# Optimization experiments

Measured on AMD Instinct MI355X. Metric: run time of the kernel, lower is better.

The kernel has to match this reference:

```python
import jax, jax.numpy as jnp
import numpy as np

D_MODEL = 1024
N_HEAD = 16
HEAD_SIZE = D_MODEL // N_HEAD
LAYER_ID = 12
N_LAYER = 24
HEAD_SIZE_DIVISOR = 8
TM_DIM = 32   # TIME_MIX_EXTRA_DIM
TD_DIM = 64   # TIME_DECAY_EXTRA_DIM
B, T = 4, 1024
EPS = 1e-5 * HEAD_SIZE_DIVISOR ** 2


def setup_inputs() -> dict:
    key = jax.random.key(0)
    ks = jax.random.split(key, 12)
    C = D_MODEL
    r0 = LAYER_ID / (N_LAYER - 1)
    r1 = 1.0 - LAYER_ID / N_LAYER
    ddd = np.arange(C, dtype=np.float64) / C
    time_maa_x = (1.0 - ddd ** r1).astype(np.float32)
    time_maa_w = (1.0 - ddd ** r1).astype(np.float32)
    time_maa_k = (1.0 - ddd ** r1).astype(np.float32)
    time_maa_v = (1.0 - (ddd ** r1 + 0.3 * r0)).astype(np.float32)
    time_maa_r = (1.0 - ddd ** (0.5 * r1)).astype(np.float32)
    time_maa_g = (1.0 - ddd ** (0.5 * r1)).astype(np.float32)
    n = np.arange(C, dtype=np.float64)
    time_decay = (-6.0 + 5.0 * (n / (C - 1)) ** (0.7 + 1.3 * r0)).astype(np.float32)
    zig = ((n + 1) % 3 - 1) * 0.1
    time_faaaa = (r0 * (1 - n / (C - 1)) + zig).astype(np.float32).reshape(N_HEAD, HEAD_SIZE)
    s = 1.0 / np.sqrt(C)
    inp = {
        "x": jax.random.normal(ks[0], (B, T, C), jnp.float32),
        "time_maa_x": jnp.asarray(time_maa_x),
        "time_maa_w": jnp.asarray(time_maa_w),
        "time_maa_k": jnp.asarray(time_maa_k),
        "time_maa_v": jnp.asarray(time_maa_v),
        "time_maa_r": jnp.asarray(time_maa_r),
        "time_maa_g": jnp.asarray(time_maa_g),
        "time_maa_w1": jax.random.uniform(ks[1], (C, TM_DIM * 5), jnp.float32, -0.01, 0.01),
        "time_maa_w2": jax.random.uniform(ks[2], (5, TM_DIM, C), jnp.float32, -0.01, 0.01),
        "time_decay": jnp.asarray(time_decay),
        "time_decay_w1": jax.random.uniform(ks[3], (C, TD_DIM), jnp.float32, -0.01, 0.01),
        "time_decay_w2": jax.random.uniform(ks[4], (TD_DIM, C), jnp.float32, -0.01, 0.01),
        "time_faaaa": jnp.asarray(time_faaaa),
        "W_r": jax.random.normal(ks[5], (C, C), jnp.float32) * s,
        "W_k": jax.random.normal(ks[6], (C, C), jnp.float32) * s,
        "W_v": jax.random.normal(ks[7], (C, C), jnp.float32) * s,
        "W_g": jax.random.normal(ks[8], (C, C), jnp.float32) * s,
        "W_o": jax.random.normal(ks[9], (C, C), jnp.float32) * s,
        "ln_gamma": jnp.ones((C,), jnp.float32),
        "ln_beta": jnp.zeros((C,), jnp.float32),
    }
    return inp


def _wkv6(r, k, v, w, u):
    # r,k,v,w: (B,T,H,K); u: (H,K). Sequential data-dependent linear attention.
    Bc, Tc, H, K = r.shape
    wdec = jnp.exp(-jnp.exp(w))  # decay in (0,1)

    def step(S, inp):
        r_t, k_t, v_t, wd_t = inp           # each (B,H,K)
        kv = k_t[:, :, :, None] * v_t[:, :, None, :]   # (B,H,K,K) key x value
        y = jnp.einsum('bhk,bhkj->bhj', r_t, S + u[None, :, :, None] * kv)
        S = S * wd_t[:, :, :, None] + kv    # decay along key dim, then accumulate
        return S, y

    S0 = jnp.zeros((Bc, H, K, K), r.dtype)
    xs = (jnp.swapaxes(r, 0, 1), jnp.swapaxes(k, 0, 1),
          jnp.swapaxes(v, 0, 1), jnp.swapaxes(wdec, 0, 1))
    _, ys = jax.lax.scan(step, S0, xs)      # ys: (T,B,H,K)
    return jnp.swapaxes(ys, 0, 1).reshape(Bc, Tc, H * K)


def reference(x, time_maa_x, time_maa_w, time_maa_k, time_maa_v, time_maa_r,
              time_maa_g, time_maa_w1, time_maa_w2, time_decay, time_decay_w1,
              time_decay_w2, time_faaaa, W_r, W_k, W_v, W_g, W_o, ln_gamma, ln_beta):
    Bc, Tc, C = x.shape
    H, K = N_HEAD, HEAD_SIZE
    # token shift: state[t] = x[t-1], zero at t=0
    xs = jnp.pad(x, ((0, 0), (1, 0), (0, 0)))[:, :-1]
    xx = xs - x
    # LoRA-style data-dependent mixing coefficients
    xxx = x + xx * time_maa_x
    m = jnp.tanh(xxx @ time_maa_w1).reshape(Bc, Tc, 5, TM_DIM)
    m = jnp.einsum('btfe,fec->fbtc', m, time_maa_w2)  # (5,B,T,C)
    mw, mk, mv, mr, mg = m[0], m[1], m[2], m[3], m[4]
    xw = x + xx * (time_maa_w + mw)
    xk = x + xx * (time_maa_k + mk)
    xv = x + xx * (time_maa_v + mv)
    xr = x + xx * (time_maa_r + mr)
    xg = x + xx * (time_maa_g + mg)
    r = xr @ W_r
    k = xk @ W_k
    v = xv @ W_v
    g = jax.nn.silu(xg @ W_g)
    w = time_decay + jnp.tanh(xw @ time_decay_w1) @ time_decay_w2
    y = _wkv6(r.reshape(Bc, Tc, H, K), k.reshape(Bc, Tc, H, K),
              v.reshape(Bc, Tc, H, K), w.reshape(Bc, Tc, H, K), time_faaaa)
    # GroupNorm with H groups over channel dim (per (b,t) position)
    yg = y.reshape(Bc, Tc, H, K)
    mu = jnp.mean(yg, axis=-1, keepdims=True)
    var = jnp.mean((yg - mu) ** 2, axis=-1, keepdims=True)
    yn = ((yg - mu) / jnp.sqrt(var + EPS)).reshape(Bc, Tc, C)
    yn = yn * ln_gamma + ln_beta
    return (yn * g) @ W_o
```

## Files before the change

### kernel.cpp

```cpp
#include <hip/hip_runtime.h>

#define Bb 4
#define Tt 1024
#define Cc 1024
#define Hh 16
#define BT (Bb*Tt)
#define CHUNK 32
#define NCH (Tt/CHUNK)

typedef unsigned int uint;
typedef unsigned short u16;
typedef __bf16 bf16x8 __attribute__((ext_vector_type(8)));
typedef float f32x4 __attribute__((ext_vector_type(4)));
typedef const __attribute__((address_space(1))) uint GU;
typedef __attribute__((address_space(3))) uint LU;

__device__ __forceinline__ float blo(uint u) { return __uint_as_float(u << 16); }
__device__ __forceinline__ float bhi(uint u) { return __uint_as_float(u & 0xffff0000u); }
__device__ __forceinline__ float b2f(u16 u) { return __uint_as_float(((uint)u) << 16); }
__device__ __forceinline__ u16 f2b(float f) {
  uint u = __float_as_uint(f);
  return (u16)((u + 0x7fffu + ((u >> 16) & 1u)) >> 16);
}

__global__ __launch_bounds__(256) void prep_xxx(const float* __restrict__ x,
    const float* __restrict__ maa_x, u16* __restrict__ xxx)
{
  int idx = blockIdx.x*256 + threadIdx.x;
  int c4 = idx & 255;
  int bt = idx >> 8;
  int t = bt & (Tt-1);
  float4 xc = ((const float4*)x)[idx];
  float4 xp = make_float4(0.f,0.f,0.f,0.f);
  if (t > 0) xp = ((const float4*)x)[idx - 256];
  float4 mx = ((const float4*)maa_x)[c4];
  ushort4 o;
  o.x = f2b(fmaf(xp.x - xc.x, mx.x, xc.x));
  o.y = f2b(fmaf(xp.y - xc.y, mx.y, xc.y));
  o.z = f2b(fmaf(xp.z - xc.z, mx.z, xc.z));
  o.w = f2b(fmaf(xp.w - xc.w, mx.w, xc.w));
  ((ushort4*)xxx)[idx] = o;
}

__global__ __launch_bounds__(256) void mix_mfma(
    const float* __restrict__ x, const u16* __restrict__ m1b,
    const u16* __restrict__ w2T,
    const float* __restrict__ maa_w, const float* __restrict__ maa_k,
    const float* __restrict__ maa_v, const float* __restrict__ maa_r,
    const float* __restrict__ maa_g,
    u16* __restrict__ xw, u16* __restrict__ xk, u16* __restrict__ xv,
    u16* __restrict__ xr, u16* __restrict__ xg)
{
  const int tid = threadIdx.x;
  const int lane = tid & 63;
  const int wv = tid >> 6;
  const int sid = blockIdx.x*4 + wv;
  const int rs = sid >> 4, cs = sid & 15;
  const int r0 = rs*16, c0 = cs*64;
  const int fr = lane & 15, kc = lane >> 4;

  float xc[4][4], xd[4][4];
  #pragma unroll
  for (int n = 0; n < 4; ++n) {
    int col = c0 + n*16 + fr;
    #pragma unroll
    for (int q = 0; q < 4; ++q) {
      int row = r0 + kc*4 + q;
      size_t o = (size_t)row*Cc + col;
      float v = x[o];
      float p = ((row & (Tt-1)) != 0) ? x[o - Cc] : 0.f;
      xc[n][q] = v;
      xd[n][q] = p - v;
    }
  }

  const u16* aB = m1b + (size_t)(r0 + fr)*160 + kc*8;
  u16* const outs[5] = {xw, xk, xv, xr, xg};
  const float* const maas[5] = {maa_w, maa_k, maa_v, maa_r, maa_g};

  #pragma unroll
  for (int f = 0; f < 5; ++f) {
    bf16x8 af = *(const bf16x8*)(aB + f*32);
    f32x4 acc[4];
    #pragma unroll
    for (int n = 0; n < 4; ++n) {
      bf16x8 bg = *(const bf16x8*)(w2T + (size_t)(c0 + n*16 + fr)*160 + f*32 + kc*8);
      acc[n] = __builtin_amdgcn_mfma_f32_16x16x32_bf16(af, bg, f32x4{0.f,0.f,0.f,0.f}, 0, 0, 0);
    }
    const float* __restrict__ ma = maas[f];
    u16* __restrict__ op = outs[f];
    #pragma unroll
    for (int n = 0; n < 4; ++n) {
      int col = c0 + n*16 + fr;
      float mv = ma[col];
      #pragma unroll
      for (int q = 0; q < 4; ++q) {
        int row = r0 + kc*4 + q;
        op[(size_t)row*Cc + col] = f2b(fmaf(xd[n][q], mv + acc[n][q], xc[n][q]));
      }
    }
  }
}

struct WPair { const float* s; u16* d; int K; int N; };
struct WPack { WPair p[9]; };

__global__ __launch_bounds__(256) void transW(WPack wp) {
  WPair pr = wp.p[blockIdx.z];
  int c0 = blockIdx.x*32, r0 = blockIdx.y*32;
  if (c0 >= pr.N || r0 >= pr.K) return;
  __shared__ float tile[32][33];
  int tc = threadIdx.x & 31, tr = threadIdx.x >> 5;
  #pragma unroll
  for (int p = 0; p < 4; ++p)
    tile[tr + p*8][tc] = pr.s[(size_t)(r0 + tr + p*8)*pr.N + c0 + tc];
  __syncthreads();
  #pragma unroll
  for (int p = 0; p < 4; ++p) {
    int n = tr + p*8;
    pr.d[(size_t)(c0 + n)*pr.K + r0 + tc] = f2b(tile[tc][n]);
  }
}

template<bool OUTF32>
__device__ __forceinline__ void mfma_core(
    const u16* __restrict__ A, const u16* __restrict__ Bt,
    void* __restrict__ Cout, const float* __restrict__ bias,
    int K, int N, int act)
{
  __shared__ __align__(16) u16 lds[2][2][128*32];
  const int tid = threadIdx.x;
  const int lane = tid & 63;
  const int wv = __builtin_amdgcn_readfirstlane(tid >> 6);

  const int nby8 = gridDim.y >> 3;
  const int i_lin = blockIdx.y * gridDim.x + blockIdx.x;
  const int cx = i_lin & 7, rest = i_lin >> 3;
  const int bm = (cx * nby8 + rest % nby8) * 128;
  const int bn = (rest / nby8) * 128;

  const int wm = (wv >> 1) * 64;
  const int wn = (wv & 1) * 64;
  const int kc = lane >> 4;
  const int fr = lane & 15;

  const int srow = wv*16 + (lane >> 2);
  const int ssw  = (srow >> 1) & 3;
  const int scol = ((lane & 3) ^ ssw) * 8;
  const size_t aoff = (size_t)(bm + srow) * K + scol;
  const size_t boff = (size_t)(bn + srow) * K + scol;

#define STAGE(bufi, kt) do { \
    size_t ko_ = (size_t)(kt) * 32; \
    __builtin_amdgcn_global_load_lds((GU*)(A + aoff + ko_), \
        (LU*)&lds[bufi][0][wv*512], 16, 0, 0); \
    __builtin_amdgcn_global_load_lds((GU*)(A + aoff + (size_t)64*K + ko_), \
        (LU*)&lds[bufi][0][wv*512 + 64*32], 16, 0, 0); \
    __builtin_amdgcn_global_load_lds((GU*)(Bt + boff + ko_), \
        (LU*)&lds[bufi][1][wv*512], 16, 0, 0); \
    __builtin_amdgcn_global_load_lds((GU*)(Bt + boff + (size_t)64*K + ko_), \
        (LU*)&lds[bufi][1][wv*512 + 64*32], 16, 0, 0); \
  } while(0)

  int ard[4], brd[4];
  #pragma unroll
  for (int m = 0; m < 4; ++m) {
    int ra = wm + m*16 + fr;
    int rb = wn + m*16 + fr;
    ard[m] = ra*32 + (kc ^ ((ra >> 1) & 3))*8;
    brd[m] = rb*32 + (kc ^ ((rb >> 1) & 3))*8;
  }

  f32x4 acc[4][4];
  #pragma unroll
  for (int m = 0; m < 4; ++m)
    #pragma unroll
    for (int n = 0; n < 4; ++n)
      acc[m][n] = f32x4{0.f, 0.f, 0.f, 0.f};

  const int NK = K >> 5;
  STAGE(0, 0);
  __syncthreads();
  int buf = 0;
  for (int kt = 0; kt < NK; ++kt) {
    if (kt + 1 < NK) STAGE(buf^1, kt+1);
    bf16x8 af[4], bg[4];
    #pragma unroll
    for (int m = 0; m < 4; ++m) af[m] = *(const bf16x8*)&lds[buf][0][ard[m]];
    #pragma unroll
    for (int n = 0; n < 4; ++n) bg[n] = *(const bf16x8*)&lds[buf][1][brd[n]];
    #pragma unroll
    for (int m = 0; m < 4; ++m)
      #pragma unroll
      for (int n = 0; n < 4; ++n)
        acc[m][n] = __builtin_amdgcn_mfma_f32_16x16x32_bf16(af[m], bg[n], acc[m][n], 0, 0, 0);
    __syncthreads();
    buf ^= 1;
  }
#undef STAGE

  const int orow = bm + wm + (lane >> 4) * 4;
  const int ocol = bn + wn + fr;
  #pragma unroll
  for (int m = 0; m < 4; ++m) {
    #pragma unroll
    for (int n = 0; n < 4; ++n) {
      int col = ocol + n*16;
      if (col < N) {
        float bs = bias ? bias[col] : 0.f;
        #pragma unroll
        for (int q = 0; q < 4; ++q) {
          float vv = acc[m][n][q] + bs;
          if (act == 1) vv = tanhf(vv);
          else if (act == 2) vv = vv / (1.f + __expf(-vv));
          else if (act == 3) vv = __expf(-__expf(vv));
          else if (act == 4) vv = __expf(vv);
          size_t off = (size_t)(orow + m*16 + q) * N + col;
          if (OUTF32) ((float*)Cout)[off] = vv;
          else ((u16*)Cout)[off] = f2b(vv);
        }
      }
    }
  }
}

template<int ACT, bool OUTF32>
__global__ __launch_bounds__(256) void gemm_mfma(
    const u16* __restrict__ A, const u16* __restrict__ Bt,
    void* __restrict__ Cout, const float* __restrict__ bias, int K, int N)
{
  mfma_core<OUTF32>(A, Bt, Cout, bias, K, N, ACT);
}

struct GPack { const u16* A[4]; const u16* B[4]; u16* C[4]; };

#define VMW(n) asm volatile("s_waitcnt vmcnt(" #n ")" ::: "memory")
#define LGKM0() asm volatile("s_waitcnt lgkmcnt(0)" ::: "memory")
#define SCHB() __builtin_amdgcn_sched_barrier(0)
#define HBAR() __builtin_amdgcn_s_barrier()

__global__ __launch_bounds__(512) void gemm_rkvg256(GPack gp) {
  __shared__ __align__(16) u16 lds[2][2][2][8192];
  const int z = blockIdx.z;
  const u16* __restrict__ Ap  = gp.A[z];
  const u16* __restrict__ Btp = gp.B[z];
  u16* __restrict__ Cp = gp.C[z];
  const int act = (z == 3) ? 2 : 0;

  const int tid = threadIdx.x;
  const int lane = tid & 63;
  const int wv = __builtin_amdgcn_readfirstlane(tid >> 6);

  const int i_lin = blockIdx.y * gridDim.x + blockIdx.x;
  const int tile = (i_lin & 7) * 8 + (i_lin >> 3);
  const int bm = (tile >> 2) * 256;
  const int bn = (tile & 3) * 256;

  const int wm = (wv >> 2) * 128;
  const int wn = (wv & 3) * 64;
  const int kc = lane >> 4;
  const int fr = lane & 15;

  const int srow0 = (wv*2 + 0)*16 + (lane >> 2);
  const int srow1 = (wv*2 + 1)*16 + (lane >> 2);
  const int sc0 = ((lane & 3) ^ ((srow0 >> 1) & 3)) * 8;
  const int sc1 = ((lane & 3) ^ ((srow1 >> 1) & 3)) * 8;
  const size_t aoff0 = (size_t)(bm + srow0)*Cc + sc0;
  const size_t aoff1 = (size_t)(bm + srow1)*Cc + sc1;
  const size_t boff0 = (size_t)(bn + srow0)*Cc + sc0;
  const size_t boff1 = (size_t)(bn + srow1)*Cc + sc1;

  int ard[8], brd[4];
  #pragma unroll
  for (int mh = 0; mh < 2; ++mh)
    #pragma unroll
    for (int mf = 0; mf < 4; ++mf) {
      int r = wm + mh*64 + mf*16 + fr;
      ard[mh*4+mf] = r*32 + (kc ^ ((r >> 1) & 3))*8;
    }
  #pragma unroll
  for (int nf = 0; nf < 4; ++nf) {
    int r = wn + nf*16 + fr;
    brd[nf] = r*32 + (kc ^ ((r >> 1) & 3))*8;
  }

  f32x4 acc[8][4];
  #pragma unroll
  for (int m = 0; m < 8; ++m)
    #pragma unroll
    for (int n = 0; n < 4; ++n)
      acc[m][n] = f32x4{0.f, 0.f, 0.f, 0.f};

#define STG256(DB, MAT, KH, kt, off0, off1, src) do { \
    u16* dst_ = &lds[(DB)][(MAT)][(KH)][wv*1024]; \
    __builtin_amdgcn_global_load_lds((GU*)((src) + (off0) + (size_t)(kt)*64 + (KH)*32), \
        (LU*)dst_, 16, 0, 0); \
    __builtin_amdgcn_global_load_lds((GU*)((src) + (off1) + (size_t)(kt)*64 + (KH)*32), \
        (LU*)(dst_ + 512), 16, 0, 0); \
  } while(0)

#define PH256(cur, KH, MH, LOADB, STMAT, STKH, DOSTAGE, VMTOK) do { \
    _Pragma("unroll") \
    for (int mf = 0; mf < 4; ++mf) \
      af[mf] = *(const bf16x8*)&lds[(cur)][0][KH][ard[(MH)*4+mf]]; \
    if (LOADB) { \
      _Pragma("unroll") \
      for (int nf = 0; nf < 4; ++nf) \
        bg[nf] = *(const bf16x8*)&lds[(cur)][1][KH][brd[nf]]; \
    } \
    if (DOSTAGE) { \
      if ((STMAT) == 0) STG256((cur)^1, 0, STKH, t+1, aoff0, aoff1, Ap); \
      else              STG256((cur)^1, 1, STKH, t+1, boff0, boff1, Btp); \
    } \
    VMTOK; \
    SCHB(); \
    HBAR(); \
    LGKM0(); \
    SCHB(); \
    __builtin_amdgcn_s_setprio(1); \
    _Pragma("unroll") \
    for (int mf = 0; mf < 4; ++mf) \
      _Pragma("unroll") \
      for (int nf = 0; nf < 4; ++nf) \
        acc[(MH)*4+mf][nf] = __builtin_amdgcn_mfma_f32_16x16x32_bf16(af[mf], bg[nf], acc[(MH)*4+mf][nf], 0, 0, 0); \
    __builtin_amdgcn_s_setprio(0); \
    SCHB(); \
    HBAR(); \
  } while(0)

  const int NK = Cc >> 6;

  STG256(0, 0, 0, 0, aoff0, aoff1, Ap);
  STG256(0, 1, 0, 0, boff0, boff1, Btp);
  STG256(0, 0, 1, 0, aoff0, aoff1, Ap);
  STG256(0, 1, 1, 0, boff0, boff1, Btp);
  VMW(4);
  SCHB();
  HBAR();

  bf16x8 af[4], bg[4];
  int t;
  #pragma unroll 2
  for (t = 0; t < NK - 1; ++t) {
    const int cur = t & 1;
    PH256(cur, 0, 0, true,  0, 0, true,  (void)0);
    PH256(cur, 0, 1, false, 1, 0, true,  VMW(4));
    PH256(cur, 1, 0, true,  0, 1, true,  (void)0);
    PH256(cur, 1, 1, false, 1, 1, true,  VMW(4));
  }
  {
    const int cur = t & 1;
    PH256(cur, 0, 0, true,  0, 0, false, (void)0);
    PH256(cur, 0, 1, false, 0, 0, false, VMW(0));
    PH256(cur, 1, 0, true,  0, 0, false, (void)0);
    PH256(cur, 1, 1, false, 0, 0, false, (void)0);
  }
#undef PH256
#undef STG256

  const int orow = bm + wm + (lane >> 4) * 4;
  const int ocol = bn + wn + fr;
  #pragma unroll
  for (int m = 0; m < 8; ++m) {
    #pragma unroll
    for (int nf = 0; nf < 4; ++nf) {
      #pragma unroll
      for (int q = 0; q < 4; ++q) {
        float vv = acc[m][nf][q];
        if (act == 2) vv = vv / (1.f + __expf(-vv));
        Cp[(size_t)(orow + (m >> 2)*64 + (m & 3)*16 + q) * Cc + ocol + nf*16] = f2b(vv);
      }
    }
  }
}

__global__ __launch_bounds__(256) void wkv_pass1(u16* __restrict__ r,
    const u16* __restrict__ k, const u16* __restrict__ v,
    const float* __restrict__ ew, const float* __restrict__ u,
    float* __restrict__ y, u16* __restrict__ S, float* __restrict__ D)
{
  __shared__ __align__(16) u16 rS[CHUNK][72];
  __shared__ __align__(16) u16 kS[CHUNK][72];
  __shared__ __align__(16) u16 vS[CHUNK][72];
  __shared__ __align__(16) float bufEW[CHUNK][68];
  __shared__ __align__(16) float eKnL[CHUNK][68];
  __shared__ __align__(16) u16 Rt[CHUNK][72];
  __shared__ __align__(16) u16 Kt[CHUNK][72];
  __shared__ __align__(16) u16 Ru[CHUNK][72];
  __shared__ __align__(16) u16 KhT[64][40];
  __shared__ __align__(16) u16 VT[64][40];
  __shared__ __align__(16) u16 A_lds[CHUNK][40];
  __shared__ float uL[64];
  __shared__ float Dl[64];

  const int blk = blockIdx.x;
  const int chunk = blk & (NCH-1);
  const int bh = blk >> 5;
  const int h = bh & (Hh-1);
  const int b = bh >> 4;
  const int tid = threadIdx.x;
  const int lane = tid & 63;
  const int wv = tid >> 6;
  const int fr = lane & 15;
  const int kc = lane >> 4;

  const size_t rowbase = ((size_t)(b*Tt + chunk*CHUNK))*Cc + h*64;
  {
    int tt = tid >> 3, c8 = (tid & 7)*8;
    size_t go = rowbase + (size_t)tt*Cc + c8;
    *(uint4*)&rS[tt][c8] = *(const uint4*)(r + go);
    *(uint4*)&kS[tt][c8] = *(const uint4*)(k + go);
    *(uint4*)&vS[tt][c8] = *(const uint4*)(v + go);
    *(float4*)&bufEW[tt][c8]   = *(const float4*)(ew + go);
    *(float4*)&bufEW[tt][c8+4] = *(const float4*)(ew + go + 4);
  }
  if (tid < 64) uL[tid] = u[h*64 + tid];
  __syncthreads();

  if (tid < 64) {
    float lwp = 0.f;
    for (int t = 0; t < CHUNK; ++t) {
      float e = bufEW[t][tid];
      bufEW[t][tid] = __expf(lwp);
      lwp -= e;
      eKnL[t][tid] = __expf(-lwp);
    }
    Dl[tid] = __expf(lwp);
    D[(size_t)blk*64 + tid] = Dl[tid];
  }
  __syncthreads();

  {
    int t = tid >> 3, i0 = (tid & 7)*8;
    uint4 rv4 = *(const uint4*)&rS[t][i0];
    uint4 kv4 = *(const uint4*)&kS[t][i0];
    const uint* rw = (const uint*)&rv4;
    const uint* kw = (const uint*)&kv4;
    u16 rt8[8], kt8[8], ru8[8];
    #pragma unroll
    for (int q = 0; q < 8; ++q) {
      int i = i0 + q;
      float rv = (q & 1) ? bhi(rw[q>>1]) : blo(rw[q>>1]);
      float kv = (q & 1) ? bhi(kw[q>>1]) : blo(kw[q>>1]);
      float eR = bufEW[t][i];
      float eKn = eKnL[t][i];
      float ktv = kv * eKn;
      rt8[q] = f2b(rv * eR);
      kt8[q] = f2b(ktv);
      ru8[q] = f2b(rv * uL[i]);
      KhT[i][t] = f2b(ktv * Dl[i]);
      VT[i][t] = vS[t][i];
    }
    *(uint4*)&Rt[t][i0] = *(const uint4*)rt8;
    *(uint4*)&Kt[t][i0] = *(const uint4*)kt8;
    *(uint4*)&Ru[t][i0] = *(const uint4*)ru8;
  }
  __syncthreads();

  {
    const int wr = wv >> 1, wc = wv & 1;
    f32x4 accA = {0.f,0.f,0.f,0.f};
    f32x4 accD = {0.f,0.f,0.f,0.f};
    #pragma unroll
    for (int ks = 0; ks < 2; ++ks) {
      bf16x8 a  = *(const bf16x8*)&Rt[wr*16+fr][kc*8 + ks*32];
      bf16x8 bb = *(const bf16x8*)&Kt[wc*16+fr][kc*8 + ks*32];
      accA = __builtin_amdgcn_mfma_f32_16x16x32_bf16(a, bb, accA, 0, 0, 0);
      bf16x8 a2 = *(const bf16x8*)&Ru[wr*16+fr][kc*8 + ks*32];
      bf16x8 b2 = *(const bf16x8*)&kS[wc*16+fr][kc*8 + ks*32];
      accD = __builtin_amdgcn_mfma_f32_16x16x32_bf16(a2, b2, accD, 0, 0, 0);
    }
    #pragma unroll
    for (int q = 0; q < 4; ++q) {
      int trow = wr*16 + kc*4 + q;
      int scol = wc*16 + fr;
      float val = (scol < trow) ? accA[q] : ((scol == trow) ? accD[q] : 0.f);
      A_lds[trow][scol] = f2b(val);
    }
  }
  __syncthreads();

  #pragma unroll
  for (int tb = 0; tb < 2; ++tb) {
    bf16x8 a  = *(const bf16x8*)&A_lds[tb*16+fr][kc*8];
    bf16x8 bb = *(const bf16x8*)&VT[wv*16+fr][kc*8];
    f32x4 acc = {0.f,0.f,0.f,0.f};
    acc = __builtin_amdgcn_mfma_f32_16x16x32_bf16(a, bb, acc, 0, 0, 0);
    #pragma unroll
    for (int q = 0; q < 4; ++q) {
      int t = tb*16 + kc*4 + q;
      int j = wv*16 + fr;
      y[rowbase + (size_t)t*Cc + j] = acc[q];
    }
  }
  #pragma unroll
  for (int jb = 0; jb < 4; ++jb) {
    bf16x8 a  = *(const bf16x8*)&KhT[wv*16+fr][kc*8];
    bf16x8 bb = *(const bf16x8*)&VT[jb*16+fr][kc*8];
    f32x4 acc = {0.f,0.f,0.f,0.f};
    acc = __builtin_amdgcn_mfma_f32_16x16x32_bf16(a, bb, acc, 0, 0, 0);
    #pragma unroll
    for (int q = 0; q < 4; ++q) {
      int i = wv*16 + kc*4 + q;
      int j = jb*16 + fr;
      S[((size_t)blk*64 + i)*64 + j] = f2b(acc[q]);
    }
  }
  {
    int tt = tid >> 3, c8 = (tid & 7)*8;
    *(uint4*)(r + rowbase + (size_t)tt*Cc + c8) = *(const uint4*)&Rt[tt][c8];
  }
}

__global__ __launch_bounds__(256) void wkv_pass2(u16* __restrict__ S,
    const float* __restrict__ D)
{
  __shared__ float Dl[NCH][64];
  const int bh = blockIdx.x;
  const int tid = threadIdx.x;
  {
    const float4* src = (const float4*)(D + (size_t)bh*NCH*64);
    float4* dst = (float4*)&Dl[0][0];
    dst[tid] = src[tid];
    dst[tid + 256] = src[tid + 256];
  }
  __syncthreads();
  const int j = tid & 63, i0 = (tid >> 6)*16;
  float Sr[16];
  #pragma unroll
  for (int ii = 0; ii < 16; ++ii) Sr[ii] = 0.f;
  for (int c = 0; c < NCH; ++c) {
    size_t base = (((size_t)bh*NCH + c)*64 + i0)*64 + j;
    u16 tmp[16];
    #pragma unroll
    for (int ii = 0; ii < 16; ++ii) tmp[ii] = S[base + ii*64];
    #pragma unroll
    for (int ii = 0; ii < 16; ++ii) S[base + ii*64] = f2b(Sr[ii]);
    #pragma unroll
    for (int ii = 0; ii < 16; ++ii) Sr[ii] = fmaf(Sr[ii], Dl[c][i0+ii], b2f(tmp[ii]));
  }
}

__global__ __launch_bounds__(256) void gn_gate(const float* __restrict__ y,
   const u16* __restrict__ g, const u16* __restrict__ rc, const u16* __restrict__ S,
   const float* __restrict__ gamma, const float* __restrict__ beta, u16* __restrict__ out)
{
  __shared__ u16 rcl[8][Cc];
  const int bt0 = blockIdx.x * 8;
  const int b = bt0 >> 10;
  const int t0 = bt0 & (Tt-1);
  const int chunk = t0 >> 5;
  const int tid = threadIdx.x;
  #pragma unroll
  for (int rr = 0; rr < 8; ++rr)
    ((ushort4*)rcl[rr])[tid] = ((const ushort4*)(rc + (size_t)(bt0+rr)*Cc))[tid];
  __syncthreads();
  const int c0 = tid*4, h = c0 >> 6, j0 = c0 & 63;
  const u16* Sb = S + (((size_t)(b*Hh + h)*NCH + chunk)*64)*64 + j0;
  float corr[8][4];
  #pragma unroll
  for (int rr = 0; rr < 8; ++rr)
    #pragma unroll
    for (int q = 0; q < 4; ++q) corr[rr][q] = 0.f;
  #pragma unroll 4
  for (int i = 0; i < 64; ++i) {
    ushort4 sv = *(const ushort4*)(Sb + (size_t)i*64);
    float s0 = b2f(sv.x), s1 = b2f(sv.y), s2 = b2f(sv.z), s3 = b2f(sv.w);
    #pragma unroll
    for (int rr = 0; rr < 8; ++rr) {
      float rv = b2f(rcl[rr][h*64 + i]);
      corr[rr][0] = fmaf(rv, s0, corr[rr][0]);
      corr[rr][1] = fmaf(rv, s1, corr[rr][1]);
      corr[rr][2] = fmaf(rv, s2, corr[rr][2]);
      corr[rr][3] = fmaf(rv, s3, corr[rr][3]);
    }
  }
  float4 ga = ((const float4*)gamma)[tid];
  float4 be = ((const float4*)beta)[tid];
  #pragma unroll
  for (int rr = 0; rr < 8; ++rr) {
    size_t o4 = (size_t)(bt0+rr)*(Cc/4) + tid;
    float4 yv = ((const float4*)y)[o4];
    yv.x += corr[rr][0]; yv.y += corr[rr][1]; yv.z += corr[rr][2]; yv.w += corr[rr][3];
    float s  = yv.x + yv.y + yv.z + yv.w;
    float sq = yv.x*yv.x + yv.y*yv.y + yv.z*yv.z + yv.w*yv.w;
    #pragma unroll
    for (int m = 1; m < 16; m <<= 1) {
      s  += __shfl_xor(s, m, 64);
      sq += __shfl_xor(sq, m, 64);
    }
    float mu  = s * (1.f/64.f);
    float var = sq * (1.f/64.f) - mu*mu;
    float rstd = rsqrtf(var + 6.4e-4f);
    ushort4 gu = ((const ushort4*)g)[o4];
    ushort4 ou;
    ou.x = f2b(((yv.x - mu)*rstd*ga.x + be.x) * b2f(gu.x));
    ou.y = f2b(((yv.y - mu)*rstd*ga.y + be.y) * b2f(gu.y));
    ou.z = f2b(((yv.z - mu)*rstd*ga.z + be.z) * b2f(gu.z));
    ou.w = f2b(((yv.w - mu)*rstd*ga.w + be.w) * b2f(gu.w));
    ((ushort4*)out)[o4] = ou;
  }
}

extern "C" void kernel_launch(void* const* d_in, const int* in_sizes, int n_in,
                              void* d_out, int out_size, void* d_ws, size_t ws_size,
                              hipStream_t stream) {
  const float* x      = (const float*)d_in[0];
  const float* maa_x  = (const float*)d_in[1];
  const float* maa_w  = (const float*)d_in[2];
  const float* maa_k  = (const float*)d_in[3];
  const float* maa_v  = (const float*)d_in[4];
  const float* maa_r  = (const float*)d_in[5];
  const float* maa_g  = (const float*)d_in[6];
  const float* w1     = (const float*)d_in[7];
  const float* w2     = (const float*)d_in[8];
  const float* tdecay = (const float*)d_in[9];
  const float* tdw1   = (const float*)d_in[10];
  const float* tdw2   = (const float*)d_in[11];
  const float* faaaa  = (const float*)d_in[12];
  const float* Wr     = (const float*)d_in[13];
  const float* Wk     = (const float*)d_in[14];
  const float* Wv     = (const float*)d_in[15];
  const float* Wg     = (const float*)d_in[16];
  const float* Wo     = (const float*)d_in[17];
  const float* gamma  = (const float*)d_in[18];
  const float* beta   = (const float*)d_in[19];
  float* out = (float*)d_out;

  const size_t MB = 1u << 20;
  char* wsb = (char*)d_ws;
  float* ewb  = (float*)(wsb + 0);
  u16*   m1b  = (u16*)(wsb + 0);
  u16*   w2T  = (u16*)(wsb + 8*MB);
  u16*   xk   = (u16*)(wsb + 16*MB);
  u16*   xv   = (u16*)(wsb + 24*MB);
  u16*   xr   = (u16*)(wsb + 32*MB);
  u16*   xg   = (u16*)(wsb + 40*MB);
  u16*   xw   = (u16*)(wsb + 48*MB);
  u16*   rbuf = (u16*)(wsb + 56*MB);
  u16*   wl1s = (u16*)(wsb + 56*MB);
  u16*   kbuf = (u16*)(wsb + 64*MB);
  u16*   vbuf = (u16*)(wsb + 72*MB);
  u16*   gbuf = (u16*)(wsb + 80*MB);
  float* Dbuf = (float*)(wsb + 88*MB);
  u16*   Sbuf = (u16*)(wsb + 16*MB);
  u16*   BW0  = (u16*)(wsb + 88*MB + 512*1024);
  u16*   BW1  = (u16*)((char*)BW0 + 2*MB);
  u16*   BW2  = (u16*)((char*)BW1 + 2*MB);
  u16*   BW3  = (u16*)((char*)BW2 + 2*MB);
  u16*   BW4  = (u16*)((char*)BW3 + 2*MB);
  u16*   w1T  = (u16*)((char*)BW4 + 2*MB);
  u16*   tdw1T = (u16*)(wsb + 99*MB);
  u16*   tdw2T = (u16*)(wsb + 99*MB + 256*1024);
  u16*   gated = xr;
  u16*   xxx16 = (u16*)d_out;
  float* ybuf  = (float*)d_out;

  dim3 blk(256);
  WPack wp;
  wp.p[0] = {Wr, BW0, Cc, Cc};  wp.p[1] = {Wk, BW1, Cc, Cc};
  wp.p[2] = {Wv, BW2, Cc, Cc};  wp.p[3] = {Wg, BW3, Cc, Cc};
  wp.p[4] = {Wo, BW4, Cc, Cc};  wp.p[5] = {w1, w1T, Cc, 160};
  wp.p[6] = {tdw1, tdw1T, Cc, 64}; wp.p[7] = {tdw2, tdw2T, 64, Cc};
  wp.p[8] = {w2, w2T, 160, Cc};
  transW<<<dim3(32,32,9), blk, 0, stream>>>(wp);
  prep_xxx<<<BT*Cc/4/256, blk, 0, stream>>>(x, maa_x, xxx16);
  gemm_mfma<1,false><<<dim3(2, 32), blk, 0, stream>>>(xxx16, w1T, m1b, nullptr, Cc, 160);
  mix_mfma<<<1024, blk, 0, stream>>>(x, m1b, w2T, maa_w, maa_k, maa_v, maa_r, maa_g,
                                     xw, xk, xv, xr, xg);
  gemm_mfma<1,false><<<dim3(1, 32), blk, 0, stream>>>(xw, tdw1T, wl1s, nullptr, Cc, 64);
  gemm_mfma<4,true><<<dim3(8, 32), blk, 0, stream>>>(wl1s, tdw2T, ewb, tdecay, 64, Cc);
  GPack gp;
  gp.A[0] = xr; gp.A[1] = xk; gp.A[2] = xv; gp.A[3] = xg;
  gp.B[0] = BW0; gp.B[1] = BW1; gp.B[2] = BW2; gp.B[3] = BW3;
  gp.C[0] = rbuf; gp.C[1] = kbuf; gp.C[2] = vbuf; gp.C[3] = gbuf;
  gemm_rkvg256<<<dim3(4, 16, 4), dim3(512), 0, stream>>>(gp);
  wkv_pass1<<<Bb*Hh*NCH, blk, 0, stream>>>(rbuf, kbuf, vbuf, ewb, faaaa, ybuf, Sbuf, Dbuf);
  wkv_pass2<<<Bb*Hh, blk, 0, stream>>>(Sbuf, Dbuf);
  gn_gate<<<BT/8, blk, 0, stream>>>(ybuf, gbuf, rbuf, Sbuf, gamma, beta, gated);
  gemm_mfma<0,true><<<dim3(8, 32), blk, 0, stream>>>(gated, BW4, out, nullptr, Cc, Cc);
}
```

Baseline: 208.6 us.

## Switch projection GEMM to 32x32x16 MFMA tiles with merged A/B staging phases

Rewrites the main projection GEMM inner loop to use 32x32x16 bf16 MFMA instructions instead of 16x16x32, with each wave holding 4x2 blocks of 32x32 accumulators. Each k-half is now one phase that loads all A and B fragments and stages both the A and B tiles for the next iteration, halving the barrier count per k-step. Larger MFMA tiles cut LDS fragment reads per FLOP, but the phase structure has less interleaving of loads and compute and may raise register pressure.

```diff
diff --git a/kernel.cpp b/kernel.cpp
--- a/kernel.cpp
+++ b/kernel.cpp
@@ -12,6 +12,7 @@
 typedef unsigned short u16;
 typedef __bf16 bf16x8 __attribute__((ext_vector_type(8)));
 typedef float f32x4 __attribute__((ext_vector_type(4)));
+typedef float f32x16 __attribute__((ext_vector_type(16)));
 typedef const __attribute__((address_space(1))) uint GU;
 typedef __attribute__((address_space(3))) uint LU;
 
@@ -258,8 +259,8 @@
 
   const int wm = (wv >> 2) * 128;
   const int wn = (wv & 3) * 64;
-  const int kc = lane >> 4;
-  const int fr = lane & 15;
+  const int l31 = lane & 31;
+  const int khi = lane >> 5;
 
   const int srow0 = (wv*2 + 0)*16 + (lane >> 2);
   const int srow1 = (wv*2 + 1)*16 + (lane >> 2);
@@ -270,26 +271,30 @@
   const size_t boff0 = (size_t)(bn + srow0)*Cc + sc0;
   const size_t boff1 = (size_t)(bn + srow1)*Cc + sc1;
 
-  int ard[8], brd[4];
-  #pragma unroll
-  for (int mh = 0; mh < 2; ++mh)
-    #pragma unroll
-    for (int mf = 0; mf < 4; ++mf) {
-      int r = wm + mh*64 + mf*16 + fr;
-      ard[mh*4+mf] = r*32 + (kc ^ ((r >> 1) & 3))*8;
-    }
-  #pragma unroll
-  for (int nf = 0; nf < 4; ++nf) {
-    int r = wn + nf*16 + fr;
-    brd[nf] = r*32 + (kc ^ ((r >> 1) & 3))*8;
-  }
-
-  f32x4 acc[8][4];
-  #pragma unroll
-  for (int m = 0; m < 8; ++m)
-    #pragma unroll
-    for (int n = 0; n < 4; ++n)
-      acc[m][n] = f32x4{0.f, 0.f, 0.f, 0.f};
+  int ard[4][2], brd[2][2];
+  #pragma unroll
+  for (int mb = 0; mb < 4; ++mb)
+    #pragma unroll
+    for (int ks = 0; ks < 2; ++ks) {
+      int r = wm + mb*32 + l31;
+      ard[mb][ks] = r*32 + ((ks*2 + khi) ^ ((r >> 1) & 3))*8;
+    }
+  #pragma unroll
+  for (int nb = 0; nb < 2; ++nb)
+    #pragma unroll
+    for (int ks = 0; ks < 2; ++ks) {
+      int r = wn + nb*32 + l31;
+      brd[nb][ks] = r*32 + ((ks*2 + khi) ^ ((r >> 1) & 3))*8;
+    }
+
+  f32x16 acc[4][2];
+  #pragma unroll
+  for (int mb = 0; mb < 4; ++mb)
+    #pragma unroll
+    for (int nb = 0; nb < 2; ++nb)
+      #pragma unroll
+      for (int q = 0; q < 16; ++q)
+        acc[mb][nb][q] = 0.f;
 
 #define STG256(DB, MAT, KH, kt, off0, off1, src) do { \
     u16* dst_ = &lds[(DB)][(MAT)][(KH)][wv*1024]; \
@@ -299,18 +304,21 @@
         (LU*)(dst_ + 512), 16, 0, 0); \
   } while(0)
 
-#define PH256(cur, KH, MH, LOADB, STMAT, STKH, DOSTAGE, VMTOK) do { \
+#define PH32(cur, KH, DOSTAGE, VMTOK) do { \
+    bf16x8 af[4][2], bg[2][2]; \
     _Pragma("unroll") \
-    for (int mf = 0; mf < 4; ++mf) \
-      af[mf] = *(const bf16x8*)&lds[(cur)][0][KH][ard[(MH)*4+mf]]; \
-    if (LOADB) { \
+    for (int mb = 0; mb < 4; ++mb) \
       _Pragma("unroll") \
-      for (int nf = 0; nf < 4; ++nf) \
-        bg[nf] = *(const bf16x8*)&lds[(cur)][1][KH][brd[nf]]; \
-    } \
+      for (int ks = 0; ks < 2; ++ks) \
+        af[mb][ks] = *(const bf16x8*)&lds[(cur)][0][KH][ard[mb][ks]]; \
+    _Pragma("unroll") \
+    for (int nb = 0; nb < 2; ++nb) \
+      _Pragma("unroll") \
+      for (int ks = 0; ks < 2; ++ks) \
+        bg[nb][ks] = *(const bf16x8*)&lds[(cur)][1][KH][brd[nb][ks]]; \
     if (DOSTAGE) { \
-      if ((STMAT) == 0) STG256((cur)^1, 0, STKH, t+1, aoff0, aoff1, Ap); \
-      else              STG256((cur)^1, 1, STKH, t+1, boff0, boff1, Btp); \
+      STG256((cur)^1, 0, KH, t+1, aoff0, aoff1, Ap); \
+      STG256((cur)^1, 1, KH, t+1, boff0, boff1, Btp); \
     } \
     VMTOK; \
     SCHB(); \
@@ -319,10 +327,12 @@
     SCHB(); \
     __builtin_amdgcn_s_setprio(1); \
     _Pragma("unroll") \
-    for (int mf = 0; mf < 4; ++mf) \
+    for (int ks = 0; ks < 2; ++ks) \
       _Pragma("unroll") \
-      for (int nf = 0; nf < 4; ++nf) \
-        acc[(MH)*4+mf][nf] = __builtin_amdgcn_mfma_f32_16x16x32_bf16(af[mf], bg[nf], acc[(MH)*4+mf][nf], 0, 0, 0); \
+      for (int mb = 0; mb < 4; ++mb) \
+        _Pragma("unroll") \
+        for (int nb = 0; nb < 2; ++nb) \
+          acc[mb][nb] = __builtin_amdgcn_mfma_f32_32x32x16_bf16(af[mb][ks], bg[nb][ks], acc[mb][nb], 0, 0, 0); \
     __builtin_amdgcn_s_setprio(0); \
     SCHB(); \
     HBAR(); \
@@ -338,37 +348,32 @@
   SCHB();
   HBAR();
 
-  bf16x8 af[4], bg[4];
   int t;
   #pragma unroll 2
   for (t = 0; t < NK - 1; ++t) {
     const int cur = t & 1;
-    PH256(cur, 0, 0, true,  0, 0, true,  (void)0);
-    PH256(cur, 0, 1, false, 1, 0, true,  VMW(4));
-    PH256(cur, 1, 0, true,  0, 1, true,  (void)0);
-    PH256(cur, 1, 1, false, 1, 1, true,  VMW(4));
+    PH32(cur, 0, true, VMW(4));
+    PH32(cur, 1, true, VMW(4));
   }
   {
     const int cur = t & 1;
-    PH256(cur, 0, 0, true,  0, 0, false, (void)0);
-    PH256(cur, 0, 1, false, 0, 0, false, VMW(0));
-    PH256(cur, 1, 0, true,  0, 0, false, (void)0);
-    PH256(cur, 1, 1, false, 0, 0, false, (void)0);
-  }
-#undef PH256
+    PH32(cur, 0, false, VMW(0));
+    PH32(cur, 1, false, (void)0);
+  }
+#undef PH32
 #undef STG256
 
-  const int orow = bm + wm + (lane >> 4) * 4;
-  const int ocol = bn + wn + fr;
-  #pragma unroll
-  for (int m = 0; m < 8; ++m) {
-    #pragma unroll
-    for (int nf = 0; nf < 4; ++nf) {
+  const int cbase = bn + wn + l31;
+  #pragma unroll
+  for (int mb = 0; mb < 4; ++mb) {
+    #pragma unroll
+    for (int nb = 0; nb < 2; ++nb) {
       #pragma unroll
-      for (int q = 0; q < 4; ++q) {
-        float vv = acc[m][nf][q];
+      for (int reg = 0; reg < 16; ++reg) {
+        int row = bm + wm + mb*32 + (reg & 3) + 8*(reg >> 2) + 4*khi;
+        float vv = acc[mb][nb][reg];
         if (act == 2) vv = vv / (1.f + __expf(-vv));
-        Cp[(size_t)(orow + (m >> 2)*64 + (m & 3)*16 + q) * Cc + ocol + nf*16] = f2b(vv);
+        Cp[(size_t)row*Cc + cbase + nb*32] = f2b(vv);
       }
     }
   }
```

After: 211.1 us. Within noise of the previous version (+1.2%).

## Split-K the skinny LoRA GEMMs and fuse partial-sum reduction with tanh into consumers

Applied to the files above, without the earlier changes.

The two narrow LoRA projections (K=1024, N=160 and N=64) previously ran on only 64 and 32 blocks. They now split K into four slices across blockIdx.z, which writes fp32 partial products. The consumers (mix_mfma and a new gemm_ew64 kernel) sum the four partials and apply tanh on load, fusing the old epilogue into the next stage. This gives the underfilled GEMMs four times more parallelism, at the cost of extra fp32 partial traffic and repeated reductions in the consumers.

```diff
diff --git a/kernel.cpp b/kernel.cpp
--- a/kernel.cpp
+++ b/kernel.cpp
@@ -43,7 +43,7 @@
 }
 
 __global__ __launch_bounds__(256) void mix_mfma(
-    const float* __restrict__ x, const u16* __restrict__ m1b,
+    const float* __restrict__ x, const float* __restrict__ m1p,
     const u16* __restrict__ w2T,
     const float* __restrict__ maa_w, const float* __restrict__ maa_k,
     const float* __restrict__ maa_v, const float* __restrict__ maa_r,
@@ -74,13 +74,24 @@
     }
   }
 
-  const u16* aB = m1b + (size_t)(r0 + fr)*160 + kc*8;
+  const size_t aBase = (size_t)(r0 + fr)*160 + kc*8;
   u16* const outs[5] = {xw, xk, xv, xr, xg};
   const float* const maas[5] = {maa_w, maa_k, maa_v, maa_r, maa_g};
 
   #pragma unroll
   for (int f = 0; f < 5; ++f) {
-    bf16x8 af = *(const bf16x8*)(aB + f*32);
+    float s8[8] = {0.f,0.f,0.f,0.f,0.f,0.f,0.f,0.f};
+    #pragma unroll
+    for (int z = 0; z < 4; ++z) {
+      const float4* p = (const float4*)(m1p + (size_t)z*655360 + aBase + f*32);
+      float4 a = p[0], b = p[1];
+      s8[0]+=a.x; s8[1]+=a.y; s8[2]+=a.z; s8[3]+=a.w;
+      s8[4]+=b.x; s8[5]+=b.y; s8[6]+=b.z; s8[7]+=b.w;
+    }
+    u16 t8[8];
+    #pragma unroll
+    for (int j = 0; j < 8; ++j) t8[j] = f2b(tanhf(s8[j]));
+    bf16x8 af = *(const bf16x8*)t8;
     f32x4 acc[4];
     #pragma unroll
     for (int n = 0; n < 4; ++n) {
@@ -126,7 +137,7 @@
 __device__ __forceinline__ void mfma_core(
     const u16* __restrict__ A, const u16* __restrict__ Bt,
     void* __restrict__ Cout, const float* __restrict__ bias,
-    int K, int N, int act)
+    int ld, int kloop, int N, int act)
 {
   __shared__ __align__(16) u16 lds[2][2][128*32];
   const int tid = threadIdx.x;
@@ -147,18 +158,18 @@
   const int srow = wv*16 + (lane >> 2);
   const int ssw  = (srow >> 1) & 3;
   const int scol = ((lane & 3) ^ ssw) * 8;
-  const size_t aoff = (size_t)(bm + srow) * K + scol;
-  const size_t boff = (size_t)(bn + srow) * K + scol;
+  const size_t aoff = (size_t)(bm + srow) * ld + scol;
+  const size_t boff = (size_t)(bn + srow) * ld + scol;
 
 #define STAGE(bufi, kt) do { \
     size_t ko_ = (size_t)(kt) * 32; \
     __builtin_amdgcn_global_load_lds((GU*)(A + aoff + ko_), \
         (LU*)&lds[bufi][0][wv*512], 16, 0, 0); \
-    __builtin_amdgcn_global_load_lds((GU*)(A + aoff + (size_t)64*K + ko_), \
+    __builtin_amdgcn_global_load_lds((GU*)(A + aoff + (size_t)64*ld + ko_), \
         (LU*)&lds[bufi][0][wv*512 + 64*32], 16, 0, 0); \
     __builtin_amdgcn_global_load_lds((GU*)(Bt + boff + ko_), \
         (LU*)&lds[bufi][1][wv*512], 16, 0, 0); \
-    __builtin_amdgcn_global_load_lds((GU*)(Bt + boff + (size_t)64*K + ko_), \
+    __builtin_amdgcn_global_load_lds((GU*)(Bt + boff + (size_t)64*ld + ko_), \
         (LU*)&lds[bufi][1][wv*512 + 64*32], 16, 0, 0); \
   } while(0)
 
@@ -178,7 +189,7 @@
     for (int n = 0; n < 4; ++n)
       acc[m][n] = f32x4{0.f, 0.f, 0.f, 0.f};
 
-  const int NK = K >> 5;
+  const int NK = kloop >> 5;
   STAGE(0, 0);
   __syncthreads();
   int buf = 0;
@@ -229,7 +240,89 @@
     const u16* __restrict__ A, const u16* __restrict__ Bt,
     void* __restrict__ Cout, const float* __restrict__ bias, int K, int N)
 {
-  mfma_core<OUTF32>(A, Bt, Cout, bias, K, N, ACT);
+  mfma_core<OUTF32>(A, Bt, Cout, bias, K, K, N, ACT);
+}
+
+__global__ __launch_bounds__(256) void gemm_ksplit(
+    const u16* __restrict__ A, const u16* __restrict__ Bt,
+    float* __restrict__ Cp, int ld, int ksz, int N)
+{
+  const int z = blockIdx.z;
+  mfma_core<true>(A + (size_t)z*ksz, Bt + (size_t)z*ksz,
+                  Cp + (size_t)z*4096*N, nullptr, ld, ksz, N, 0);
+}
+
+__global__ __launch_bounds__(256) void gemm_ew64(
+    const float* __restrict__ wl1p, const u16* __restrict__ Bt,
+    const float* __restrict__ tdecay, float* __restrict__ ew)
+{
+  const int tid = threadIdx.x;
+  const int lane = tid & 63;
+  const int wv = tid >> 6;
+  const int nby8 = gridDim.y >> 3;
+  const int i_lin = blockIdx.y * gridDim.x + blockIdx.x;
+  const int cx = i_lin & 7, rest = i_lin >> 3;
+  const int bm = (cx * nby8 + rest % nby8) * 128;
+  const int bn = (rest / nby8) * 128;
+  const int wm = (wv >> 1) * 64;
+  const int wn = (wv & 1) * 64;
+  const int kc = lane >> 4;
+  const int fr = lane & 15;
+
+  bf16x8 af[4][2];
+  #pragma unroll
+  for (int m = 0; m < 4; ++m) {
+    int row = bm + wm + m*16 + fr;
+    #pragma unroll
+    for (int ks = 0; ks < 2; ++ks) {
+      size_t base = (size_t)row*64 + ks*32 + kc*8;
+      float s8[8] = {0.f,0.f,0.f,0.f,0.f,0.f,0.f,0.f};
+      #pragma unroll
+      for (int z = 0; z < 4; ++z) {
+        const float4* p = (const float4*)(wl1p + (size_t)z*262144 + base);
+        float4 a = p[0], b = p[1];
+        s8[0]+=a.x; s8[1]+=a.y; s8[2]+=a.z; s8[3]+=a.w;
+        s8[4]+=b.x; s8[5]+=b.y; s8[6]+=b.z; s8[7]+=b.w;
+      }
+      u16 t8[8];
+      #pragma unroll
+      for (int j = 0; j < 8; ++j) t8[j] = f2b(tanhf(s8[j]));
+      af[m][ks] = *(const bf16x8*)t8;
+    }
+  }
+
+  f32x4 acc[4][4];
+  #pragma unroll
+  for (int m = 0; m < 4; ++m)
+    #pragma unroll
+    for (int n = 0; n < 4; ++n)
+      acc[m][n] = f32x4{0.f,0.f,0.f,0.f};
+
+  #pragma unroll
+  for (int ks = 0; ks < 2; ++ks) {
+    bf16x8 bg[4];
+    #pragma unroll
+    for (int n = 0; n < 4; ++n)
+      bg[n] = *(const bf16x8*)(Bt + (size_t)(bn + wn + n*16 + fr)*64 + ks*32 + kc*8);
+    #pragma unroll
+    for (int m = 0; m < 4; ++m)
+      #pragma unroll
+      for (int n = 0; n < 4; ++n)
+        acc[m][n] = __builtin_amdgcn_mfma_f32_16x16x32_bf16(af[m][ks], bg[n], acc[m][n], 0, 0, 0);
+  }
+
+  const int orow = bm + wm + kc*4;
+  const int ocol = bn + wn + fr;
+  #pragma unroll
+  for (int n = 0; n < 4; ++n) {
+    int col = ocol + n*16;
+    float bs = tdecay[col];
+    #pragma unroll
+    for (int m = 0; m < 4; ++m)
+      #pragma unroll
+      for (int q = 0; q < 4; ++q)
+        ew[(size_t)(orow + m*16 + q)*Cc + col] = __expf(acc[m][n][q] + bs);
+  }
 }
 
 struct GPack { const u16* A[4]; const u16* B[4]; u16* C[4]; };
@@ -630,15 +723,15 @@
   const size_t MB = 1u << 20;
   char* wsb = (char*)d_ws;
   float* ewb  = (float*)(wsb + 0);
-  u16*   m1b  = (u16*)(wsb + 0);
-  u16*   w2T  = (u16*)(wsb + 8*MB);
+  float* m1p  = (float*)(wsb + 0);
+  u16*   w2T  = (u16*)(wsb + 12*MB);
   u16*   xk   = (u16*)(wsb + 16*MB);
   u16*   xv   = (u16*)(wsb + 24*MB);
   u16*   xr   = (u16*)(wsb + 32*MB);
   u16*   xg   = (u16*)(wsb + 40*MB);
   u16*   xw   = (u16*)(wsb + 48*MB);
   u16*   rbuf = (u16*)(wsb + 56*MB);
-  u16*   wl1s = (u16*)(wsb + 56*MB);
+  float* wl1p = (float*)(wsb + 56*MB);
   u16*   kbuf = (u16*)(wsb + 64*MB);
   u16*   vbuf = (u16*)(wsb + 72*MB);
   u16*   gbuf = (u16*)(wsb + 80*MB);
@@ -665,11 +758,11 @@
   wp.p[8] = {w2, w2T, 160, Cc};
   transW<<<dim3(32,32,9), blk, 0, stream>>>(wp);
   prep_xxx<<<BT*Cc/4/256, blk, 0, stream>>>(x, maa_x, xxx16);
-  gemm_mfma<1,false><<<dim3(2, 32), blk, 0, stream>>>(xxx16, w1T, m1b, nullptr, Cc, 160);
-  mix_mfma<<<1024, blk, 0, stream>>>(x, m1b, w2T, maa_w, maa_k, maa_v, maa_r, maa_g,
+  gemm_ksplit<<<dim3(2, 32, 4), blk, 0, stream>>>(xxx16, w1T, m1p, Cc, 256, 160);
+  mix_mfma<<<1024, blk, 0, stream>>>(x, m1p, w2T, maa_w, maa_k, maa_v, maa_r, maa_g,
                                      xw, xk, xv, xr, xg);
-  gemm_mfma<1,false><<<dim3(1, 32), blk, 0, stream>>>(xw, tdw1T, wl1s, nullptr, Cc, 64);
-  gemm_mfma<4,true><<<dim3(8, 32), blk, 0, stream>>>(wl1s, tdw2T, ewb, tdecay, 64, Cc);
+  gemm_ksplit<<<dim3(1, 32, 4), blk, 0, stream>>>(xw, tdw1T, wl1p, Cc, 256, 64);
+  gemm_ew64<<<dim3(8, 32), blk, 0, stream>>>(wl1p, tdw2T, tdecay, ewb);
   GPack gp;
   gp.A[0] = xr; gp.A[1] = xk; gp.A[2] = xv; gp.A[3] = xg;
   gp.B[0] = BW0; gp.B[1] = BW1; gp.B[2] = BW2; gp.B[3] = BW3;
```

After: 200.3 us. 1.04x faster.
